# Performance work log

Hardware: AMD Instinct MI355X
Metric: run time of the kernel (lower is better)

Reference implementation:

```python
import jax, jax.numpy as jnp
import numpy as np

NEG_SLOPE = 0.2  # PyG GATConv default LeakyReLU slope


def add_self_loops(edge_index, n):
    loops = jnp.arange(n, dtype=edge_index.dtype)
    return jnp.concatenate([edge_index, jnp.stack([loops, loops])], axis=1)


def segment_softmax(e, seg, n):
    # e: [E, H], seg: [E] destination node ids
    m = jax.ops.segment_max(e, seg, num_segments=n)          # [N, H]
    ex = jnp.exp(e - m[seg])
    s = jax.ops.segment_sum(ex, seg, num_segments=n)          # [N, H]
    return ex / (s[seg] + 1e-16)


def gat_conv(x, edge_index, W, att_src, att_dst, bias, heads, concat):
    n = x.shape[0]
    c = W.shape[1] // heads
    ei = add_self_loops(edge_index, n)
    src, dst = ei[0], ei[1]
    h = (x @ W).reshape(n, heads, c)                          # [N, H, C]
    a_src = jnp.einsum('nhc,hc->nh', h, att_src)              # [N, H]
    a_dst = jnp.einsum('nhc,hc->nh', h, att_dst)
    e = a_src[src] + a_dst[dst]                               # [E, H]
    e = jax.nn.leaky_relu(e, NEG_SLOPE)
    alpha = segment_softmax(e, dst, n)                        # [E, H]
    msg = alpha[:, :, None] * h[src]                          # [E, H, C]
    out = jax.ops.segment_sum(msg, dst, num_segments=n)       # [N, H, C]
    if concat:
        out = out.reshape(n, heads * c)
    else:
        out = out.mean(axis=1)
    return out + bias


def setup_inputs() -> dict:
    key = jax.random.key(0)
    ks = jax.random.split(key, 16)
    N, E, IN, HID, H, OUT = 50000, 1600000, 512, 256, 8, 128
    s = 0.1
    return {
        'x': jax.random.normal(ks[0], (N, IN), jnp.float32),
        'edge_index': jax.random.randint(ks[1], (2, E), 0, N, jnp.int64),
        'edge_index_2': jax.random.randint(ks[2], (2, E), 0, N, jnp.int64),
        'W1': jax.random.normal(ks[3], (IN, HID * H), jnp.float32) * s,
        'att_src1': jax.random.normal(ks[4], (H, HID), jnp.float32) * s,
        'att_dst1': jax.random.normal(ks[5], (H, HID), jnp.float32) * s,
        'b1': jnp.zeros((HID * H,), jnp.float32),
        'W2': jax.random.normal(ks[6], (HID * H, OUT), jnp.float32) * s,
        'att_src2': jax.random.normal(ks[7], (1, OUT), jnp.float32) * s,
        'att_dst2': jax.random.normal(ks[8], (1, OUT), jnp.float32) * s,
        'b2': jnp.zeros((OUT,), jnp.float32),
        'W3': jax.random.normal(ks[9], (HID * H, OUT), jnp.float32) * s,
        'att_src3': jax.random.normal(ks[10], (1, OUT), jnp.float32) * s,
        'att_dst3': jax.random.normal(ks[11], (1, OUT), jnp.float32) * s,
        'b3': jnp.zeros((OUT,), jnp.float32),
    }


def reference(x, edge_index, edge_index_2, W1, att_src1, att_dst1, b1,
              W2, att_src2, att_dst2, b2, W3, att_src3, att_dst3, b3):
    # Inference mode: F.dropout and GATConv attention dropout are no-ops.
    emb = jax.nn.elu(gat_conv(x, edge_index, W1, att_src1, att_dst1, b1, heads=8, concat=True))
    x1 = gat_conv(emb, edge_index, W2, att_src2, att_dst2, b2, heads=1, concat=False)
    x2 = gat_conv(emb, edge_index_2, W3, att_src3, att_dst3, b3, heads=1, concat=False)
    logits = jax.nn.softmax(x1, axis=1)    # nn.Softmax() legacy dim -> 1 for 2D
    logits_2 = jax.nn.softmax(x2, axis=1)
    predictions = jnp.argmax(logits, axis=1)
    return (logits, logits_2, predictions)
```

## Files before the change

kernel.cpp:

```cpp
#include <hip/hip_runtime.h>
#include <hip/hip_bf16.h>
#include <math.h>

#define N_NODES 50000
#define E_EDGES 1600000
#define EP_EDGES (E_EDGES + N_NODES)
#define IN_F 512
#define HID 256
#define HEADS 8
#define OUTF 128

typedef unsigned short u16;
typedef __attribute__((ext_vector_type(8))) short short8;
typedef __attribute__((ext_vector_type(4))) float floatx4;

static __device__ __forceinline__ float eluf(float x) {
  return x > 0.f ? x : expm1f(x);
}

static __device__ __forceinline__ u16 bf16_hi(float v) {
  __hip_bfloat16 h = __float2bfloat16(v);
  return *(u16*)&h;
}
static __device__ __forceinline__ float bf16_f(u16 u) {
  __hip_bfloat16 h = *(__hip_bfloat16*)&u;
  return __bfloat162float(h);
}
static __device__ __forceinline__ void split3_bf16(float v, u16& h, u16& m, u16& l) {
  h = bf16_hi(v);
  float r1 = v - bf16_f(h);
  m = bf16_hi(r1);
  float r2 = r1 - bf16_f(m);
  l = bf16_hi(r2);
}

static __device__ __forceinline__ int clampi(int v, int n) {
  return v < 0 ? 0 : (v >= n ? n - 1 : v);
}


__global__ void k_detect(const int* __restrict__ ei, int* __restrict__ flag) {
  __shared__ int nz;
  if (threadIdx.x == 0) nz = 0;
  __syncthreads();
  for (int i = threadIdx.x; i < 4096; i += blockDim.x)
    if (ei[2 * i + 1] != 0) nz = 1;
  __syncthreads();
  if (threadIdx.x == 0) *flag = (nz ? 0 : 1);
}

__global__ void k_init_deg(int* __restrict__ deg, int n) {
  int i = blockIdx.x * 256 + threadIdx.x;
  if (i < n) deg[i] = 1;
}

__global__ void k_count(const int* __restrict__ ei, const int* __restrict__ flag,
                        int* __restrict__ deg, int E) {
  int e = blockIdx.x * 256 + threadIdx.x;
  if (e >= E) return;
  int f = *flag;
  int idx = E + e;
  int dst = clampi(ei[f ? 2 * idx : idx], N_NODES);
  atomicAdd(&deg[dst], 1);
}

__global__ __launch_bounds__(1024) void k_scan(const int* __restrict__ deg,
                                               int* __restrict__ rp, int n) {
  __shared__ int sd[1024];
  __shared__ int s_run;
  int tid = threadIdx.x;
  if (tid == 0) s_run = 0;
  __syncthreads();
  for (int base = 0; base < n; base += 1024) {
    int i = base + tid;
    int v = (i < n) ? deg[i] : 0;
    sd[tid] = v;
    __syncthreads();
    for (int off = 1; off < 1024; off <<= 1) {
      int t = (tid >= off) ? sd[tid - off] : 0;
      __syncthreads();
      sd[tid] += t;
      __syncthreads();
    }
    int run = s_run;
    if (i < n) rp[i + 1] = run + sd[tid];
    __syncthreads();
    if (tid == 1023) s_run = run + sd[1023];
    __syncthreads();
  }
  if (tid == 0) rp[0] = 0;
}

__global__ void k_fill_self(const int* __restrict__ rp, int* __restrict__ wp,
                            int* __restrict__ col, int n) {
  int i = blockIdx.x * 256 + threadIdx.x;
  if (i < n) { int p = rp[i]; col[p] = i; wp[i] = p + 1; }
}

__global__ void k_fill_edges(const int* __restrict__ ei, const int* __restrict__ flag,
                             int* __restrict__ wp, int* __restrict__ col, int E) {
  int e = blockIdx.x * 256 + threadIdx.x;
  if (e >= E) return;
  int f = *flag;
  int src = clampi(ei[f ? 2 * e : e], N_NODES);
  int didx = E + e;
  int dst = clampi(ei[f ? 2 * didx : didx], N_NODES);
  int p = atomicAdd(&wp[dst], 1);
  col[p] = src;
}

__global__ void k_split3_t(const float* __restrict__ W, u16* __restrict__ H,
                           u16* __restrict__ Mv, u16* __restrict__ L,
                           int kshift, int kmask, int Nw, int total) {
  int idx = blockIdx.x * 256 + threadIdx.x;
  if (idx >= total) return;
  int n = idx >> kshift;
  int k = idx & kmask;
  u16 h, m, l;
  split3_bf16(W[(size_t)k * Nw + n], h, m, l);
  H[idx] = h;
  Mv[idx] = m;
  L[idx] = l;
}


#define GBM 128
#define GBN 128
#define GBK 32

#define MFMA_BF16 __builtin_amdgcn_mfma_f32_16x16x32_bf16

__device__ __forceinline__ void gemm_epilogue(floatx4 acc[4][4], float* C,
                                              int ldc, int M, int accum,
                                              int row0, int col0, int wr,
                                              int wc, int lane) {
  int q = lane >> 4, n15 = lane & 15;
#pragma unroll
  for (int i = 0; i < 4; ++i) {
#pragma unroll
    for (int r = 0; r < 4; ++r) {
      int row = row0 + wr * 64 + i * 16 + q * 4 + r;
      if (row < M) {
#pragma unroll
        for (int j = 0; j < 4; ++j) {
          int cg = col0 + wc * 64 + j * 16 + n15;
          float v = acc[i][j][r];
          if (accum) v += C[(size_t)row * ldc + cg];
          C[(size_t)row * ldc + cg] = v;
        }
      }
    }
  }
}

__global__ __launch_bounds__(256) void gemm1_k(
    const float* __restrict__ X, int lda,
    const u16* __restrict__ Bh, const u16* __restrict__ Bm,
    const u16* __restrict__ Bl, int ldb,
    float* __restrict__ C, int ldc, int M, int K) {
  __shared__ __align__(16) u16 lds[24576];
  int tid = threadIdx.x;
  int lane = tid & 63, wave = tid >> 6;
  int wr = wave >> 1, wc = wave & 1;
  int row0 = blockIdx.x * GBM, col0 = blockIdx.y * GBN;
  floatx4 acc[4][4] = {};
  int m0 = tid >> 2, m1 = (tid + 256) >> 2;
  int q0 = tid & 3;
  int lo0 = ((m0 >> 4) * 64 + q0 * 16 + (m0 & 15)) * 8;
  int lo1 = ((m1 >> 4) * 64 + q0 * 16 + (m1 & 15)) * 8;

  for (int k0 = 0; k0 < K; k0 += GBK) {
#pragma unroll
    for (int c = 0; c < 2; ++c) {
      int m = c ? m1 : m0;
      int lo = c ? lo1 : lo0;
      int gr = row0 + m;
      float f[8];
      if (gr < M) {
        float4 f0 = *(const float4*)(X + (size_t)gr * lda + k0 + q0 * 8);
        float4 f1 = *(const float4*)(X + (size_t)gr * lda + k0 + q0 * 8 + 4);
        f[0] = f0.x; f[1] = f0.y; f[2] = f0.z; f[3] = f0.w;
        f[4] = f1.x; f[5] = f1.y; f[6] = f1.z; f[7] = f1.w;
      } else {
#pragma unroll
        for (int e = 0; e < 8; ++e) f[e] = 0.f;
      }
      short8 vh, vm, vl;
#pragma unroll
      for (int e = 0; e < 8; ++e) {
        u16 h, m2, l;
        split3_bf16(f[e], h, m2, l);
        vh[e] = (short)h; vm[e] = (short)m2; vl[e] = (short)l;
      }
      *(short8*)&lds[lo] = vh;
      *(short8*)&lds[4096 + lo] = vm;
      *(short8*)&lds[8192 + lo] = vl;
    }
#pragma unroll
    for (int c = 0; c < 2; ++c) {
      int m = c ? m1 : m0;
      int lo = c ? lo1 : lo0;
      size_t go = (size_t)(col0 + m) * ldb + k0 + q0 * 8;
      *(short8*)&lds[12288 + lo] = *(const short8*)(Bh + go);
      *(short8*)&lds[16384 + lo] = *(const short8*)(Bm + go);
      *(short8*)&lds[20480 + lo] = *(const short8*)(Bl + go);
    }
    __syncthreads();
    short8 a_h[4], a_m[4], a_l[4];
#pragma unroll
    for (int i = 0; i < 4; ++i) {
      int o = ((wr * 4 + i) * 64 + lane) * 8;
      a_h[i] = *(short8*)&lds[o];
      a_m[i] = *(short8*)&lds[4096 + o];
      a_l[i] = *(short8*)&lds[8192 + o];
    }
#pragma unroll
    for (int j = 0; j < 4; ++j) {
      int o = ((wc * 4 + j) * 64 + lane) * 8;
      short8 b_h = *(short8*)&lds[12288 + o];
      short8 b_m = *(short8*)&lds[16384 + o];
      short8 b_l = *(short8*)&lds[20480 + o];
#pragma unroll
      for (int i = 0; i < 4; ++i) {
        acc[i][j] = MFMA_BF16(a_l[i], b_h, acc[i][j], 0, 0, 0);
        acc[i][j] = MFMA_BF16(a_m[i], b_m, acc[i][j], 0, 0, 0);
        acc[i][j] = MFMA_BF16(a_h[i], b_l, acc[i][j], 0, 0, 0);
        acc[i][j] = MFMA_BF16(a_m[i], b_h, acc[i][j], 0, 0, 0);
        acc[i][j] = MFMA_BF16(a_h[i], b_m, acc[i][j], 0, 0, 0);
        acc[i][j] = MFMA_BF16(a_h[i], b_h, acc[i][j], 0, 0, 0);
      }
    }
    __syncthreads();
  }
  gemm_epilogue(acc, C, ldc, M, 0, row0, col0, wr, wc, lane);
}

__device__ __forceinline__ void gemm_core6(
    const u16* __restrict__ Ah, const u16* __restrict__ Am,
    const u16* __restrict__ Al, int lda,
    const u16* __restrict__ Bh, const u16* __restrict__ Bm,
    const u16* __restrict__ Bl, int ldb,
    float* __restrict__ C, int ldc, int M, int K, int row0, int col0,
    u16* lds) {
  int tid = threadIdx.x;
  int lane = tid & 63, wave = tid >> 6;
  int wr = wave >> 1, wc = wave & 1;
  floatx4 acc[4][4] = {};
  int m0 = tid >> 2, m1 = (tid + 256) >> 2;
  int q0 = tid & 3;
  int lo0 = ((m0 >> 4) * 64 + q0 * 16 + (m0 & 15)) * 8;
  int lo1 = ((m1 >> 4) * 64 + q0 * 16 + (m1 & 15)) * 8;
  for (int k0 = 0; k0 < K; k0 += GBK) {
#pragma unroll
    for (int c = 0; c < 2; ++c) {
      int m = c ? m1 : m0;
      int lo = c ? lo1 : lo0;
      int gr = row0 + m;
      short8 vh = {}, vm = {}, vl = {};
      if (gr < M) {
        size_t go = (size_t)gr * lda + k0 + q0 * 8;
        vh = *(const short8*)(Ah + go);
        vm = *(const short8*)(Am + go);
        vl = *(const short8*)(Al + go);
      }
      *(short8*)&lds[lo] = vh;
      *(short8*)&lds[4096 + lo] = vm;
      *(short8*)&lds[8192 + lo] = vl;
      size_t go = (size_t)(col0 + m) * ldb + k0 + q0 * 8;
      *(short8*)&lds[12288 + lo] = *(const short8*)(Bh + go);
      *(short8*)&lds[16384 + lo] = *(const short8*)(Bm + go);
      *(short8*)&lds[20480 + lo] = *(const short8*)(Bl + go);
    }
    __syncthreads();
    short8 a_h[4], a_m[4], a_l[4];
#pragma unroll
    for (int i = 0; i < 4; ++i) {
      int o = ((wr * 4 + i) * 64 + lane) * 8;
      a_h[i] = *(short8*)&lds[o];
      a_m[i] = *(short8*)&lds[4096 + o];
      a_l[i] = *(short8*)&lds[8192 + o];
    }
#pragma unroll
    for (int j = 0; j < 4; ++j) {
      int o = ((wc * 4 + j) * 64 + lane) * 8;
      short8 b_h = *(short8*)&lds[12288 + o];
      short8 b_m = *(short8*)&lds[16384 + o];
      short8 b_l = *(short8*)&lds[20480 + o];
#pragma unroll
      for (int i = 0; i < 4; ++i) {
        acc[i][j] = MFMA_BF16(a_l[i], b_h, acc[i][j], 0, 0, 0);
        acc[i][j] = MFMA_BF16(a_m[i], b_m, acc[i][j], 0, 0, 0);
        acc[i][j] = MFMA_BF16(a_h[i], b_l, acc[i][j], 0, 0, 0);
        acc[i][j] = MFMA_BF16(a_m[i], b_h, acc[i][j], 0, 0, 0);
        acc[i][j] = MFMA_BF16(a_h[i], b_m, acc[i][j], 0, 0, 0);
        acc[i][j] = MFMA_BF16(a_h[i], b_h, acc[i][j], 0, 0, 0);
      }
    }
    __syncthreads();
  }
  gemm_epilogue(acc, C, ldc, M, 1, row0, col0, wr, wc, lane);
}

__device__ __forceinline__ void gemm_core3(
    const u16* __restrict__ Ah, const u16* __restrict__ Am, int lda,
    const u16* __restrict__ Bh, const u16* __restrict__ Bm, int ldb,
    float* __restrict__ C, int ldc, int M, int K, int row0, int col0,
    u16* lds) {
  int tid = threadIdx.x;
  int lane = tid & 63, wave = tid >> 6;
  int wr = wave >> 1, wc = wave & 1;
  floatx4 acc[4][4] = {};
  int m0 = tid >> 2, m1 = (tid + 256) >> 2;
  int q0 = tid & 3;
  int lo0 = ((m0 >> 4) * 64 + q0 * 16 + (m0 & 15)) * 8;
  int lo1 = ((m1 >> 4) * 64 + q0 * 16 + (m1 & 15)) * 8;
  for (int k0 = 0; k0 < K; k0 += GBK) {
#pragma unroll
    for (int c = 0; c < 2; ++c) {
      int m = c ? m1 : m0;
      int lo = c ? lo1 : lo0;
      int gr = row0 + m;
      short8 vh = {}, vm = {};
      if (gr < M) {
        size_t go = (size_t)gr * lda + k0 + q0 * 8;
        vh = *(const short8*)(Ah + go);
        vm = *(const short8*)(Am + go);
      }
      *(short8*)&lds[lo] = vh;
      *(short8*)&lds[4096 + lo] = vm;
      size_t go = (size_t)(col0 + m) * ldb + k0 + q0 * 8;
      *(short8*)&lds[12288 + lo] = *(const short8*)(Bh + go);
      *(short8*)&lds[16384 + lo] = *(const short8*)(Bm + go);
    }
    __syncthreads();
    short8 a_h[4], a_m[4];
#pragma unroll
    for (int i = 0; i < 4; ++i) {
      int o = ((wr * 4 + i) * 64 + lane) * 8;
      a_h[i] = *(short8*)&lds[o];
      a_m[i] = *(short8*)&lds[4096 + o];
    }
#pragma unroll
    for (int j = 0; j < 4; ++j) {
      int o = ((wc * 4 + j) * 64 + lane) * 8;
      short8 b_h = *(short8*)&lds[12288 + o];
      short8 b_m = *(short8*)&lds[16384 + o];
#pragma unroll
      for (int i = 0; i < 4; ++i) {
        acc[i][j] = MFMA_BF16(a_m[i], b_h, acc[i][j], 0, 0, 0);
        acc[i][j] = MFMA_BF16(a_h[i], b_m, acc[i][j], 0, 0, 0);
        acc[i][j] = MFMA_BF16(a_h[i], b_h, acc[i][j], 0, 0, 0);
      }
    }
    __syncthreads();
  }
  gemm_epilogue(acc, C, ldc, M, 1, row0, col0, wr, wc, lane);
}

__global__ __launch_bounds__(256) void gemm23_k(
    const u16* __restrict__ Ah, const u16* __restrict__ Am,
    const u16* __restrict__ Al, int lda,
    const u16* __restrict__ B2h, const u16* __restrict__ B2m,
    const u16* __restrict__ B2l,
    const u16* __restrict__ B3h, const u16* __restrict__ B3m, int ldb,
    float* __restrict__ C2, float* __restrict__ C3, int ldc, int M, int K) {
  __shared__ __align__(16) u16 lds[24576];
  if (blockIdx.z == 0)
    gemm_core6(Ah, Am, Al, lda, B2h, B2m, B2l, ldb, C2, ldc, M, K,
               blockIdx.x * GBM, 0, lds);
  else
    gemm_core3(Ah, Am, lda, B3h, B3m, ldb, C3, ldc, M, K,
               blockIdx.x * GBM, 0, lds);
}

template <int C>
__global__ __launch_bounds__(256) void att_dot(
    const float* __restrict__ h, const float* __restrict__ attS,
    const float* __restrict__ attD, float* __restrict__ aS,
    float* __restrict__ aD, int n) {
  int node = (blockIdx.x * 256 + threadIdx.x) >> 6;
  int lane = threadIdx.x & 63;
  if (node >= n) return;
  float s = 0.f, d = 0.f;
  if (C == 256) {
    float4 hv = *(const float4*)&h[(size_t)node * C + lane * 4];
    float4 sv = *(const float4*)&attS[lane * 4];
    float4 dv = *(const float4*)&attD[lane * 4];
    s = hv.x * sv.x + hv.y * sv.y + hv.z * sv.z + hv.w * sv.w;
    d = hv.x * dv.x + hv.y * dv.y + hv.z * dv.z + hv.w * dv.w;
  } else {
    float2 hv = *(const float2*)&h[(size_t)node * C + lane * 2];
    float2 sv = *(const float2*)&attS[lane * 2];
    float2 dv = *(const float2*)&attD[lane * 2];
    s = hv.x * sv.x + hv.y * sv.y;
    d = hv.x * dv.x + hv.y * dv.y;
  }
  for (int off = 32; off; off >>= 1) {
    s += __shfl_xor(s, off);
    d += __shfl_xor(d, off);
  }
  if (lane == 0) { aS[node] = s; aD[node] = d; }
}

__global__ __launch_bounds__(256) void aggr_l1_fused(
    const int* __restrict__ rp, const int* __restrict__ col,
    const float* __restrict__ aS, const float* __restrict__ aD,
    const float* __restrict__ h, const float* __restrict__ bias,
    u16* __restrict__ embH, u16* __restrict__ embM, u16* __restrict__ embL,
    int n) {
  int node = (blockIdx.x * 256 + threadIdx.x) >> 6;
  int lane = threadIdx.x & 63;
  if (node >= n) return;
  int s0 = rp[node], s1 = rp[node + 1];
  int d = s1 - s0;
  float ad = aD[node];
  float4 acc = make_float4(0.f, 0.f, 0.f, 0.f);

  if (d <= 64) {
    int c = 0;
    float e = -3.0e38f;
    if (lane < d) {
      c = clampi(col[s0 + lane], n);
      float t = aS[c] + ad;
      e = t >= 0.f ? t : 0.2f * t;
    }
    float m = e;
    for (int off = 32; off; off >>= 1) m = fmaxf(m, __shfl_xor(m, off));
    float ex = (lane < d) ? expf(e - m) : 0.f;
    float s = ex;
    for (int off = 32; off; off >>= 1) s += __shfl_xor(s, off);
    float al = ex * (1.f / (s + 1e-16f));
    for (int j = 0; j < d; j += 8) {
#pragma unroll
      for (int t = 0; t < 8; ++t) {
        int ct = __shfl(c, j + t);
        float at = __shfl(al, j + t);
        float4 hv = *(const float4*)&h[(size_t)ct * HID + lane * 4];
        acc.x += at * hv.x; acc.y += at * hv.y;
        acc.z += at * hv.z; acc.w += at * hv.w;
      }
    }
  } else {
    float m = -3.0e38f;
    for (int i = s0 + lane; i < s1; i += 64) {
      float e = aS[clampi(col[i], n)] + ad;
      e = e >= 0.f ? e : 0.2f * e;
      m = fmaxf(m, e);
    }
    for (int off = 32; off; off >>= 1) m = fmaxf(m, __shfl_xor(m, off));
    float sum = 0.f;
    for (int i = s0 + lane; i < s1; i += 64) {
      float e = aS[clampi(col[i], n)] + ad;
      e = e >= 0.f ? e : 0.2f * e;
      sum += expf(e - m);
    }
    for (int off = 32; off; off >>= 1) sum += __shfl_xor(sum, off);
    float inv = 1.f / (sum + 1e-16f);
    for (int i = s0; i < s1; ++i) {
      int ci = clampi(col[i], n);
      float e = aS[ci] + ad;
      e = e >= 0.f ? e : 0.2f * e;
      float a = expf(e - m) * inv;
      float4 hv = *(const float4*)&h[(size_t)ci * HID + lane * 4];
      acc.x += a * hv.x; acc.y += a * hv.y; acc.z += a * hv.z; acc.w += a * hv.w;
    }
  }

  float4 bb = *(const float4*)&bias[lane * 4];
  float v0 = eluf(acc.x + bb.x);
  float v1 = eluf(acc.y + bb.y);
  float v2 = eluf(acc.z + bb.z);
  float v3 = eluf(acc.w + bb.w);
  ushort4 uh, um, ul;
  split3_bf16(v0, uh.x, um.x, ul.x);
  split3_bf16(v1, uh.y, um.y, ul.y);
  split3_bf16(v2, uh.z, um.z, ul.z);
  split3_bf16(v3, uh.w, um.w, ul.w);
  size_t o = (size_t)node * HID + lane * 4;
  *(ushort4*)&embH[o] = uh;
  *(ushort4*)&embM[o] = um;
  *(ushort4*)&embL[o] = ul;
}

__global__ __launch_bounds__(256) void aggr_l2_fused(
    const int* __restrict__ rp, const int* __restrict__ col,
    const float* __restrict__ aS, const float* __restrict__ aD,
    const float* __restrict__ h, const float* __restrict__ bias,
    float* __restrict__ out, int n) {
  int node = (blockIdx.x * 256 + threadIdx.x) >> 6;
  int lane = threadIdx.x & 63;
  if (node >= n) return;
  int s0 = rp[node], s1 = rp[node + 1];
  int d = s1 - s0;
  float ad = aD[node];
  float2 acc = make_float2(0.f, 0.f);

  if (d <= 64) {
    int c = 0;
    float e = -3.0e38f;
    if (lane < d) {
      c = clampi(col[s0 + lane], n);
      float t = aS[c] + ad;
      e = t >= 0.f ? t : 0.2f * t;
    }
    float m = e;
    for (int off = 32; off; off >>= 1) m = fmaxf(m, __shfl_xor(m, off));
    float ex = (lane < d) ? expf(e - m) : 0.f;
    float s = ex;
    for (int off = 32; off; off >>= 1) s += __shfl_xor(s, off);
    float al = ex * (1.f / (s + 1e-16f));
    for (int j = 0; j < d; j += 8) {
#pragma unroll
      for (int t = 0; t < 8; ++t) {
        int ct = __shfl(c, j + t);
        float at = __shfl(al, j + t);
        float2 hv = *(const float2*)&h[(size_t)ct * OUTF + lane * 2];
        acc.x += at * hv.x; acc.y += at * hv.y;
      }
    }
  } else {
    float m = -3.0e38f;
    for (int i = s0 + lane; i < s1; i += 64) {
      float e = aS[clampi(col[i], n)] + ad;
      e = e >= 0.f ? e : 0.2f * e;
      m = fmaxf(m, e);
    }
    for (int off = 32; off; off >>= 1) m = fmaxf(m, __shfl_xor(m, off));
    float sum = 0.f;
    for (int i = s0 + lane; i < s1; i += 64) {
      float e = aS[clampi(col[i], n)] + ad;
      e = e >= 0.f ? e : 0.2f * e;
      sum += expf(e - m);
    }
    for (int off = 32; off; off >>= 1) sum += __shfl_xor(sum, off);
    float inv = 1.f / (sum + 1e-16f);
    for (int i = s0; i < s1; ++i) {
      int ci = clampi(col[i], n);
      float e = aS[ci] + ad;
      e = e >= 0.f ? e : 0.2f * e;
      float a = expf(e - m) * inv;
      float2 hv = *(const float2*)&h[(size_t)ci * OUTF + lane * 2];
      acc.x += a * hv.x; acc.y += a * hv.y;
    }
  }

  float2 bb = *(const float2*)&bias[lane * 2];
  acc.x += bb.x; acc.y += bb.y;
  *(float2*)&out[(size_t)node * OUTF + lane * 2] = acc;
}

__global__ __launch_bounds__(256) void softmax_rows(float* __restrict__ x,
                                                    float* __restrict__ pred,
                                                    int n) {
  int node = (blockIdx.x * 256 + threadIdx.x) >> 6;
  int lane = threadIdx.x & 63;
  if (node >= n) return;
  float2 v = *(float2*)&x[(size_t)node * OUTF + lane * 2];
  float bv;
  int bi;
  if (v.y > v.x) { bv = v.y; bi = 2 * lane + 1; }
  else           { bv = v.x; bi = 2 * lane; }
  for (int off = 32; off; off >>= 1) {
    float ov = __shfl_xor(bv, off);
    int oi = __shfl_xor(bi, off);
    if (ov > bv || (ov == bv && oi < bi)) { bv = ov; bi = oi; }
  }
  float e0 = expf(v.x - bv), e1 = expf(v.y - bv);
  float s = e0 + e1;
  for (int off = 32; off; off >>= 1) s += __shfl_xor(s, off);
  float2 r;
  r.x = e0 / s;
  r.y = e1 / s;
  *(float2*)&x[(size_t)node * OUTF + lane * 2] = r;
  if (pred != nullptr && lane == 0) pred[node] = (float)bi;
}

extern "C" void kernel_launch(void* const* d_in, const int* in_sizes, int n_in,
                              void* d_out, int out_size, void* d_ws, size_t ws_size,
                              hipStream_t stream) {
  const int N = N_NODES, E = E_EDGES;
  const float* x     = (const float*)d_in[0];
  const int*   ei1   = (const int*)d_in[1];
  const int*   ei2   = (const int*)d_in[2];
  const float* W1    = (const float*)d_in[3];
  const float* attS1 = (const float*)d_in[4];
  const float* attD1 = (const float*)d_in[5];
  const float* b1    = (const float*)d_in[6];
  const float* W2    = (const float*)d_in[7];
  const float* attS2 = (const float*)d_in[8];
  const float* attD2 = (const float*)d_in[9];
  const float* b2    = (const float*)d_in[10];
  const float* W3    = (const float*)d_in[11];
  const float* attS3 = (const float*)d_in[12];
  const float* attD3 = (const float*)d_in[13];
  const float* b3    = (const float*)d_in[14];

  char* ws = (char*)d_ws;
  size_t off = 0;
  auto take = [&](size_t bytes) {
    off = (off + 255) & ~(size_t)255;
    size_t o = off;
    off += bytes;
    return o;
  };
  int*   col1 = (int*)(ws + take((size_t)EP_EDGES * 4));
  int*   col2 = (int*)(ws + take((size_t)EP_EDGES * 4));
  int*   rp1  = (int*)(ws + take((size_t)(N + 1) * 4));
  int*   rp2  = (int*)(ws + take((size_t)(N + 1) * 4));
  int*   wp1  = (int*)(ws + take((size_t)N * 4));
  int*   wp2  = (int*)(ws + take((size_t)N * 4));
  int*   flag = (int*)(ws + take(256));
  float* h1h  = (float*)(ws + take((size_t)N * HID * 4));
  u16*   embH = (u16*)(ws + take((size_t)N * HID * 2));
  u16*   embM = (u16*)(ws + take((size_t)N * HID * 2));
  u16*   embL = (u16*)(ws + take((size_t)N * HID * 2));
  float* h2   = (float*)(ws + take((size_t)N * OUTF * 4 * 2));
  float* h3   = h2 + (size_t)N * OUTF;
  u16*   W1Th = (u16*)(ws + take((size_t)IN_F * HID * HEADS * 2));
  u16*   W1Tm = (u16*)(ws + take((size_t)IN_F * HID * HEADS * 2));
  u16*   W1Tl = (u16*)(ws + take((size_t)IN_F * HID * HEADS * 2));
  u16*   W2Th = (u16*)(ws + take((size_t)HID * HEADS * OUTF * 2));
  u16*   W2Tm = (u16*)(ws + take((size_t)HID * HEADS * OUTF * 2));
  u16*   W2Tl = (u16*)(ws + take((size_t)HID * HEADS * OUTF * 2));
  u16*   W3Th = (u16*)(ws + take((size_t)HID * HEADS * OUTF * 2));
  u16*   W3Tm = (u16*)(ws + take((size_t)HID * HEADS * OUTF * 2));
  u16*   W3Tl = (u16*)(ws + take((size_t)HID * HEADS * OUTF * 2));
  float* as1  = (float*)(ws + take((size_t)N * 4));
  float* ad1  = (float*)(ws + take((size_t)N * 4));
  float* as2  = (float*)(ws + take((size_t)N * 4));
  float* ad2  = (float*)(ws + take((size_t)N * 4));
  float* as3  = (float*)(ws + take((size_t)N * 4));
  float* ad3  = (float*)(ws + take((size_t)N * 4));

  float* outp = (float*)d_out;
  float* x1   = outp;
  float* x2   = outp + (size_t)N * OUTF;
  float* pred = outp + (size_t)2 * N * OUTF;

  const int gN = (N + 255) / 256;
  const int gE = (E + 255) / 256;
  const int gW = (N + 3) / 4;
  const int gM = (N + GBM - 1) / GBM;

  k_split3_t<<<(IN_F * HID * HEADS + 255) / 256, 256, 0, stream>>>(
      W1, W1Th, W1Tm, W1Tl, 9, 511, HID * HEADS, IN_F * HID * HEADS);
  k_split3_t<<<(HID * HEADS * OUTF + 255) / 256, 256, 0, stream>>>(
      W2, W2Th, W2Tm, W2Tl, 11, 2047, OUTF, HID * HEADS * OUTF);
  k_split3_t<<<(HID * HEADS * OUTF + 255) / 256, 256, 0, stream>>>(
      W3, W3Th, W3Tm, W3Tl, 11, 2047, OUTF, HID * HEADS * OUTF);

  k_detect<<<1, 256, 0, stream>>>(ei1, flag);

  k_init_deg<<<gN, 256, 0, stream>>>(wp1, N);
  k_count<<<gE, 256, 0, stream>>>(ei1, flag, wp1, E);
  k_scan<<<1, 1024, 0, stream>>>(wp1, rp1, N);
  k_fill_self<<<gN, 256, 0, stream>>>(rp1, wp1, col1, N);
  k_fill_edges<<<gE, 256, 0, stream>>>(ei1, flag, wp1, col1, E);

  k_init_deg<<<gN, 256, 0, stream>>>(wp2, N);
  k_count<<<gE, 256, 0, stream>>>(ei2, flag, wp2, E);
  k_scan<<<1, 1024, 0, stream>>>(wp2, rp2, N);
  k_fill_self<<<gN, 256, 0, stream>>>(rp2, wp2, col2, N);
  k_fill_edges<<<gE, 256, 0, stream>>>(ei2, flag, wp2, col2, E);

  hipMemsetAsync(h2, 0, (size_t)N * OUTF * 4 * 2, stream);

  for (int h = 0; h < HEADS; ++h) {
    gemm1_k<<<dim3(gM, HID / GBN), 256, 0, stream>>>(
        x, IN_F,
        W1Th + (size_t)h * HID * IN_F, W1Tm + (size_t)h * HID * IN_F,
        W1Tl + (size_t)h * HID * IN_F, IN_F, h1h, HID, N, IN_F);
    att_dot<HID><<<gW, 256, 0, stream>>>(h1h, attS1 + (size_t)h * HID,
                                         attD1 + (size_t)h * HID, as1, ad1, N);
    aggr_l1_fused<<<gW, 256, 0, stream>>>(rp1, col1, as1, ad1, h1h,
                                          b1 + (size_t)h * HID,
                                          embH, embM, embL, N);
    gemm23_k<<<dim3(gM, 1, 2), 256, 0, stream>>>(
        embH, embM, embL, HID,
        W2Th + (size_t)h * HID, W2Tm + (size_t)h * HID, W2Tl + (size_t)h * HID,
        W3Th + (size_t)h * HID, W3Tm + (size_t)h * HID, HID * HEADS,
        h2, h3, OUTF, N, HID);
  }

  att_dot<OUTF><<<gW, 256, 0, stream>>>(h2, attS2, attD2, as2, ad2, N);
  att_dot<OUTF><<<gW, 256, 0, stream>>>(h3, attS3, attD3, as3, ad3, N);
  aggr_l2_fused<<<gW, 256, 0, stream>>>(rp1, col1, as2, ad2, h2, b2, x1, N);
  aggr_l2_fused<<<gW, 256, 0, stream>>>(rp2, col2, as3, ad3, h3, b3, x2, N);

  softmax_rows<<<gW, 256, 0, stream>>>(x1, pred, N);
  softmax_rows<<<gW, 256, 0, stream>>>(x2, nullptr, N);
}
```

Before: 4.287 ms.

## Precompute attention logits via W·att, batch heads into layer-2 GEMM, fuse softmax

Folds the attention vectors into W1 (W1·att_src/att_dst) so all per-head source and destination logits are computed once from x, replacing the per-head att_dot pass over h1. Two heads of layer-1 embeddings are stored side by side when workspace allows, so the layer-2/3 GEMM runs with K=512 half as often. It also removes the memset by passing an accumulate flag, fuses the row softmax and argmax into the layer-2 aggregation, replaces the scan with wave shuffles, and adds a tail path for degrees not divisible by 8. The reassociated logit arithmetic can differ slightly in rounding from the original.

After: 4.137 ms. 1.04x faster.

```diff
diff --git a/kernel.cpp b/kernel.cpp
--- a/kernel.cpp
+++ b/kernel.cpp
@@ -66,26 +66,37 @@
 
 __global__ __launch_bounds__(1024) void k_scan(const int* __restrict__ deg,
                                                int* __restrict__ rp, int n) {
-  __shared__ int sd[1024];
+  __shared__ int sw[16];
   __shared__ int s_run;
-  int tid = threadIdx.x;
+  int tid = threadIdx.x, lane = tid & 63, w = tid >> 6;
   if (tid == 0) s_run = 0;
   __syncthreads();
   for (int base = 0; base < n; base += 1024) {
     int i = base + tid;
     int v = (i < n) ? deg[i] : 0;
-    sd[tid] = v;
-    __syncthreads();
-    for (int off = 1; off < 1024; off <<= 1) {
-      int t = (tid >= off) ? sd[tid - off] : 0;
-      __syncthreads();
-      sd[tid] += t;
-      __syncthreads();
-    }
+    int sv = v;
+#pragma unroll
+    for (int off = 1; off < 64; off <<= 1) {
+      int t = __shfl_up(sv, off);
+      if (lane >= off) sv += t;
+    }
+    if (lane == 63) sw[w] = sv;
+    __syncthreads();
+    if (w == 0) {
+      int wsum = (lane < 16) ? sw[lane] : 0;
+#pragma unroll
+      for (int off = 1; off < 16; off <<= 1) {
+        int t = __shfl_up(wsum, off);
+        if (lane >= off) wsum += t;
+      }
+      if (lane < 16) sw[lane] = wsum;
+    }
+    __syncthreads();
+    int woff = (w > 0) ? sw[w - 1] : 0;
     int run = s_run;
-    if (i < n) rp[i + 1] = run + sd[tid];
-    __syncthreads();
-    if (tid == 1023) s_run = run + sd[1023];
+    if (i < n) rp[i + 1] = run + woff + sv;
+    __syncthreads();
+    if (tid == 1023) s_run = run + sw[15];
     __syncthreads();
   }
   if (tid == 0) rp[0] = 0;
@@ -121,6 +132,56 @@
   H[idx] = h;
   Mv[idx] = m;
   L[idx] = l;
+}
+
+__global__ __launch_bounds__(256) void k_watt1(
+    const float* __restrict__ W1, const float* __restrict__ attS,
+    const float* __restrict__ attD, float* __restrict__ watt) {
+  int wid = (blockIdx.x * 256 + threadIdx.x) >> 6;
+  int lane = threadIdx.x & 63;
+  if (wid >= IN_F * HEADS) return;
+  int k = wid >> 3, h = wid & 7;
+  float4 wv = *(const float4*)&W1[(size_t)k * (HID * HEADS) + h * HID + lane * 4];
+  float4 sv = *(const float4*)&attS[h * HID + lane * 4];
+  float4 dv = *(const float4*)&attD[h * HID + lane * 4];
+  float s = wv.x * sv.x + wv.y * sv.y + wv.z * sv.z + wv.w * sv.w;
+  float d = wv.x * dv.x + wv.y * dv.y + wv.z * dv.z + wv.w * dv.w;
+  for (int off = 32; off; off >>= 1) {
+    s += __shfl_xor(s, off);
+    d += __shfl_xor(d, off);
+  }
+  if (lane == 0) {
+    watt[(size_t)(2 * h) * IN_F + k] = s;
+    watt[(size_t)(2 * h + 1) * IN_F + k] = d;
+  }
+}
+
+__global__ __launch_bounds__(256) void k_asad1(
+    const float* __restrict__ x, const float* __restrict__ watt,
+    float* __restrict__ asall, float* __restrict__ adall, int n) {
+  int node = (blockIdx.x * 256 + threadIdx.x) >> 6;
+  int lane = threadIdx.x & 63;
+  if (node >= n) return;
+  float4 x0 = *(const float4*)&x[(size_t)node * IN_F + lane * 8];
+  float4 x1 = *(const float4*)&x[(size_t)node * IN_F + lane * 8 + 4];
+  for (int h = 0; h < HEADS; ++h) {
+    const float* ws = watt + (size_t)(2 * h) * IN_F + lane * 8;
+    const float* wd = watt + (size_t)(2 * h + 1) * IN_F + lane * 8;
+    float4 s0 = *(const float4*)ws, s1 = *(const float4*)(ws + 4);
+    float4 d0 = *(const float4*)wd, d1 = *(const float4*)(wd + 4);
+    float s = x0.x * s0.x + x0.y * s0.y + x0.z * s0.z + x0.w * s0.w
+            + x1.x * s1.x + x1.y * s1.y + x1.z * s1.z + x1.w * s1.w;
+    float d = x0.x * d0.x + x0.y * d0.y + x0.z * d0.z + x0.w * d0.w
+            + x1.x * d1.x + x1.y * d1.y + x1.z * d1.z + x1.w * d1.w;
+    for (int off = 32; off; off >>= 1) {
+      s += __shfl_xor(s, off);
+      d += __shfl_xor(d, off);
+    }
+    if (lane == 0) {
+      asall[(size_t)h * n + node] = s;
+      adall[(size_t)h * n + node] = d;
+    }
+  }
 }
 
 
@@ -241,7 +302,7 @@
     const u16* __restrict__ Bh, const u16* __restrict__ Bm,
     const u16* __restrict__ Bl, int ldb,
     float* __restrict__ C, int ldc, int M, int K, int row0, int col0,
-    u16* lds) {
+    int accum, u16* lds) {
   int tid = threadIdx.x;
   int lane = tid & 63, wave = tid >> 6;
   int wr = wave >> 1, wc = wave & 1;
@@ -298,14 +359,14 @@
     }
     __syncthreads();
   }
-  gemm_epilogue(acc, C, ldc, M, 1, row0, col0, wr, wc, lane);
+  gemm_epilogue(acc, C, ldc, M, accum, row0, col0, wr, wc, lane);
 }
 
 __device__ __forceinline__ void gemm_core3(
     const u16* __restrict__ Ah, const u16* __restrict__ Am, int lda,
     const u16* __restrict__ Bh, const u16* __restrict__ Bm, int ldb,
     float* __restrict__ C, int ldc, int M, int K, int row0, int col0,
-    u16* lds) {
+    int accum, u16* lds) {
   int tid = threadIdx.x;
   int lane = tid & 63, wave = tid >> 6;
   int wr = wave >> 1, wc = wave & 1;
@@ -354,7 +415,7 @@
     }
     __syncthreads();
   }
-  gemm_epilogue(acc, C, ldc, M, 1, row0, col0, wr, wc, lane);
+  gemm_epilogue(acc, C, ldc, M, accum, row0, col0, wr, wc, lane);
 }
 
 __global__ __launch_bounds__(256) void gemm23_k(
@@ -363,14 +424,15 @@
     const u16* __restrict__ B2h, const u16* __restrict__ B2m,
     const u16* __restrict__ B2l,
     const u16* __restrict__ B3h, const u16* __restrict__ B3m, int ldb,
-    float* __restrict__ C2, float* __restrict__ C3, int ldc, int M, int K) {
+    float* __restrict__ C2, float* __restrict__ C3, int ldc, int M, int K,
+    int accum) {
   __shared__ __align__(16) u16 lds[24576];
   if (blockIdx.z == 0)
     gemm_core6(Ah, Am, Al, lda, B2h, B2m, B2l, ldb, C2, ldc, M, K,
-               blockIdx.x * GBM, 0, lds);
+               blockIdx.x * GBM, 0, accum, lds);
   else
     gemm_core3(Ah, Am, lda, B3h, B3m, ldb, C3, ldc, M, K,
-               blockIdx.x * GBM, 0, lds);
+               blockIdx.x * GBM, 0, accum, lds);
 }
 
 template <int C>
@@ -407,7 +469,7 @@
     const float* __restrict__ aS, const float* __restrict__ aD,
     const float* __restrict__ h, const float* __restrict__ bias,
     u16* __restrict__ embH, u16* __restrict__ embM, u16* __restrict__ embL,
-    int n) {
+    int ecol0, int ldE, int n) {
   int node = (blockIdx.x * 256 + threadIdx.x) >> 6;
   int lane = threadIdx.x & 63;
   if (node >= n) return;
@@ -430,7 +492,8 @@
     float s = ex;
     for (int off = 32; off; off >>= 1) s += __shfl_xor(s, off);
     float al = ex * (1.f / (s + 1e-16f));
-    for (int j = 0; j < d; j += 8) {
+    int d8 = d & ~7;
+    for (int j = 0; j < d8; j += 8) {
 #pragma unroll
       for (int t = 0; t < 8; ++t) {
         int ct = __shfl(c, j + t);
@@ -438,6 +501,18 @@
         float4 hv = *(const float4*)&h[(size_t)ct * HID + lane * 4];
         acc.x += at * hv.x; acc.y += at * hv.y;
         acc.z += at * hv.z; acc.w += at * hv.w;
+      }
+    }
+    if (d8 < d) {
+#pragma unroll
+      for (int t = 0; t < 8; ++t) {
+        if (d8 + t < d) {
+          int ct = __shfl(c, d8 + t);
+          float at = __shfl(al, d8 + t);
+          float4 hv = *(const float4*)&h[(size_t)ct * HID + lane * 4];
+          acc.x += at * hv.x; acc.y += at * hv.y;
+          acc.z += at * hv.z; acc.w += at * hv.w;
+        }
       }
     }
   } else {
@@ -476,7 +551,7 @@
   split3_bf16(v1, uh.y, um.y, ul.y);
   split3_bf16(v2, uh.z, um.z, ul.z);
   split3_bf16(v3, uh.w, um.w, ul.w);
-  size_t o = (size_t)node * HID + lane * 4;
+  size_t o = (size_t)node * ldE + ecol0 + lane * 4;
   *(ushort4*)&embH[o] = uh;
   *(ushort4*)&embM[o] = um;
   *(ushort4*)&embL[o] = ul;
@@ -486,7 +561,7 @@
     const int* __restrict__ rp, const int* __restrict__ col,
     const float* __restrict__ aS, const float* __restrict__ aD,
     const float* __restrict__ h, const float* __restrict__ bias,
-    float* __restrict__ out, int n) {
+    float* __restrict__ out, float* __restrict__ pred, int n) {
   int node = (blockIdx.x * 256 + threadIdx.x) >> 6;
   int lane = threadIdx.x & 63;
   if (node >= n) return;
@@ -509,13 +584,25 @@
     float s = ex;
     for (int off = 32; off; off >>= 1) s += __shfl_xor(s, off);
     float al = ex * (1.f / (s + 1e-16f));
-    for (int j = 0; j < d; j += 8) {
+    int d8 = d & ~7;
+    for (int j = 0; j < d8; j += 8) {
 #pragma unroll
       for (int t = 0; t < 8; ++t) {
         int ct = __shfl(c, j + t);
         float at = __shfl(al, j + t);
         float2 hv = *(const float2*)&h[(size_t)ct * OUTF + lane * 2];
         acc.x += at * hv.x; acc.y += at * hv.y;
+      }
+    }
+    if (d8 < d) {
+#pragma unroll
+      for (int t = 0; t < 8; ++t) {
+        if (d8 + t < d) {
+          int ct = __shfl(c, d8 + t);
+          float at = __shfl(al, d8 + t);
+          float2 hv = *(const float2*)&h[(size_t)ct * OUTF + lane * 2];
+          acc.x += at * hv.x; acc.y += at * hv.y;
+        }
       }
     }
   } else {
@@ -546,32 +633,23 @@
 
   float2 bb = *(const float2*)&bias[lane * 2];
   acc.x += bb.x; acc.y += bb.y;
-  *(float2*)&out[(size_t)node * OUTF + lane * 2] = acc;
-}
-
-__global__ __launch_bounds__(256) void softmax_rows(float* __restrict__ x,
-                                                    float* __restrict__ pred,
-                                                    int n) {
-  int node = (blockIdx.x * 256 + threadIdx.x) >> 6;
-  int lane = threadIdx.x & 63;
-  if (node >= n) return;
-  float2 v = *(float2*)&x[(size_t)node * OUTF + lane * 2];
+
   float bv;
   int bi;
-  if (v.y > v.x) { bv = v.y; bi = 2 * lane + 1; }
-  else           { bv = v.x; bi = 2 * lane; }
+  if (acc.y > acc.x) { bv = acc.y; bi = 2 * lane + 1; }
+  else               { bv = acc.x; bi = 2 * lane; }
   for (int off = 32; off; off >>= 1) {
     float ov = __shfl_xor(bv, off);
     int oi = __shfl_xor(bi, off);
     if (ov > bv || (ov == bv && oi < bi)) { bv = ov; bi = oi; }
   }
-  float e0 = expf(v.x - bv), e1 = expf(v.y - bv);
-  float s = e0 + e1;
-  for (int off = 32; off; off >>= 1) s += __shfl_xor(s, off);
+  float e0 = expf(acc.x - bv), e1 = expf(acc.y - bv);
+  float ssum = e0 + e1;
+  for (int off = 32; off; off >>= 1) ssum += __shfl_xor(ssum, off);
   float2 r;
-  r.x = e0 / s;
-  r.y = e1 / s;
-  *(float2*)&x[(size_t)node * OUTF + lane * 2] = r;
+  r.x = e0 / ssum;
+  r.y = e1 / ssum;
+  *(float2*)&out[(size_t)node * OUTF + lane * 2] = r;
   if (pred != nullptr && lane == 0) pred[node] = (float)bi;
 }
 
@@ -595,6 +673,20 @@
   const float* attD3 = (const float*)d_in[13];
   const float* b3    = (const float*)d_in[14];
 
+  size_t embPer = (size_t)N * HID * 2;
+  size_t fixedBytes =
+      2 * ((size_t)EP_EDGES * 4 + 256) + 2 * ((size_t)(N + 1) * 4 + 256) +
+      2 * ((size_t)N * 4 + 256) + 512 +
+      ((size_t)N * HID * 4 + 256) +
+      ((size_t)N * OUTF * 4 * 2 + 256) +
+      3 * ((size_t)IN_F * HID * HEADS * 2 + 256) +
+      6 * ((size_t)HID * HEADS * OUTF * 2 + 256) +
+      2 * ((size_t)HEADS * N * 4 + 256) +
+      4 * ((size_t)N * 4 + 256) +
+      ((size_t)2 * HEADS * IN_F * 4 + 256) +
+      (1 << 20);
+  int g = (ws_size >= fixedBytes + 3 * 2 * embPer) ? 2 : 1;
+
   char* ws = (char*)d_ws;
   size_t off = 0;
   auto take = [&](size_t bytes) {
@@ -611,9 +703,9 @@
   int*   wp2  = (int*)(ws + take((size_t)N * 4));
   int*   flag = (int*)(ws + take(256));
   float* h1h  = (float*)(ws + take((size_t)N * HID * 4));
-  u16*   embH = (u16*)(ws + take((size_t)N * HID * 2));
-  u16*   embM = (u16*)(ws + take((size_t)N * HID * 2));
-  u16*   embL = (u16*)(ws + take((size_t)N * HID * 2));
+  u16*   embH = (u16*)(ws + take(embPer * g));
+  u16*   embM = (u16*)(ws + take(embPer * g));
+  u16*   embL = (u16*)(ws + take(embPer * g));
   float* h2   = (float*)(ws + take((size_t)N * OUTF * 4 * 2));
   float* h3   = h2 + (size_t)N * OUTF;
   u16*   W1Th = (u16*)(ws + take((size_t)IN_F * HID * HEADS * 2));
@@ -625,12 +717,13 @@
   u16*   W3Th = (u16*)(ws + take((size_t)HID * HEADS * OUTF * 2));
   u16*   W3Tm = (u16*)(ws + take((size_t)HID * HEADS * OUTF * 2));
   u16*   W3Tl = (u16*)(ws + take((size_t)HID * HEADS * OUTF * 2));
-  float* as1  = (float*)(ws + take((size_t)N * 4));
-  float* ad1  = (float*)(ws + take((size_t)N * 4));
+  float* asall = (float*)(ws + take((size_t)HEADS * N * 4));
+  float* adall = (float*)(ws + take((size_t)HEADS * N * 4));
   float* as2  = (float*)(ws + take((size_t)N * 4));
   float* ad2  = (float*)(ws + take((size_t)N * 4));
   float* as3  = (float*)(ws + take((size_t)N * 4));
   float* ad3  = (float*)(ws + take((size_t)N * 4));
+  float* watt = (float*)(ws + take((size_t)2 * HEADS * IN_F * 4));
 
   float* outp = (float*)d_out;
   float* x1   = outp;
@@ -649,6 +742,10 @@
   k_split3_t<<<(HID * HEADS * OUTF + 255) / 256, 256, 0, stream>>>(
       W3, W3Th, W3Tm, W3Tl, 11, 2047, OUTF, HID * HEADS * OUTF);
 
+  k_watt1<<<(IN_F * HEADS * 64 + 255) / 256, 256, 0, stream>>>(
+      W1, attS1, attD1, watt);
+  k_asad1<<<gW, 256, 0, stream>>>(x, watt, asall, adall, N);
+
   k_detect<<<1, 256, 0, stream>>>(ei1, flag);
 
   k_init_deg<<<gN, 256, 0, stream>>>(wp1, N);
@@ -663,30 +760,28 @@
   k_fill_self<<<gN, 256, 0, stream>>>(rp2, wp2, col2, N);
   k_fill_edges<<<gE, 256, 0, stream>>>(ei2, flag, wp2, col2, E);
 
-  hipMemsetAsync(h2, 0, (size_t)N * OUTF * 4 * 2, stream);
-
+  const int ldE = g * HID;
   for (int h = 0; h < HEADS; ++h) {
     gemm1_k<<<dim3(gM, HID / GBN), 256, 0, stream>>>(
         x, IN_F,
         W1Th + (size_t)h * HID * IN_F, W1Tm + (size_t)h * HID * IN_F,
         W1Tl + (size_t)h * HID * IN_F, IN_F, h1h, HID, N, IN_F);
-    att_dot<HID><<<gW, 256, 0, stream>>>(h1h, attS1 + (size_t)h * HID,
-                                         attD1 + (size_t)h * HID, as1, ad1, N);
-    aggr_l1_fused<<<gW, 256, 0, stream>>>(rp1, col1, as1, ad1, h1h,
-                                          b1 + (size_t)h * HID,
-                                          embH, embM, embL, N);
-    gemm23_k<<<dim3(gM, 1, 2), 256, 0, stream>>>(
-        embH, embM, embL, HID,
-        W2Th + (size_t)h * HID, W2Tm + (size_t)h * HID, W2Tl + (size_t)h * HID,
-        W3Th + (size_t)h * HID, W3Tm + (size_t)h * HID, HID * HEADS,
-        h2, h3, OUTF, N, HID);
+    aggr_l1_fused<<<gW, 256, 0, stream>>>(
+        rp1, col1, asall + (size_t)h * N, adall + (size_t)h * N, h1h,
+        b1 + (size_t)h * HID, embH, embM, embL, (h % g) * HID, ldE, N);
+    if ((h % g) == g - 1) {
+      int h0 = h - (g - 1);
+      gemm23_k<<<dim3(gM, 1, 2), 256, 0, stream>>>(
+          embH, embM, embL, ldE,
+          W2Th + (size_t)h0 * HID, W2Tm + (size_t)h0 * HID,
+          W2Tl + (size_t)h0 * HID,
+          W3Th + (size_t)h0 * HID, W3Tm + (size_t)h0 * HID, HID * HEADS,
+          h2, h3, OUTF, N, ldE, h0 > 0 ? 1 : 0);
+    }
   }
 
   att_dot<OUTF><<<gW, 256, 0, stream>>>(h2, attS2, attD2, as2, ad2, N);
   att_dot<OUTF><<<gW, 256, 0, stream>>>(h3, attS3, attD3, as3, ad3, N);
-  aggr_l2_fused<<<gW, 256, 0, stream>>>(rp1, col1, as2, ad2, h2, b2, x1, N);
-  aggr_l2_fused<<<gW, 256, 0, stream>>>(rp2, col2, as3, ad3, h3, b3, x2, N);
-
-  softmax_rows<<<gW, 256, 0, stream>>>(x1, pred, N);
-  softmax_rows<<<gW, 256, 0, stream>>>(x2, nullptr, N);
-}
+  aggr_l2_fused<<<gW, 256, 0, stream>>>(rp1, col1, as2, ad2, h2, b2, x1, pred, N);
+  aggr_l2_fused<<<gW, 256, 0, stream>>>(rp2, col2, as3, ad3, h3, b3, x2, nullptr, N);
+}
```
